# Performance work log

Measured on AMD Instinct MI355X. Metric: run time of the kernel, lower is better.

Reference implementation:

```python
import jax, jax.numpy as jnp
import numpy as np

NUM_HEADS = 8

def _proj(x, w, b):
    # 1x1x1 Conv3d == pointwise linear over channel dim
    return jnp.einsum('bcxyz,oc->boxyz', x, w) + b[None, :, None, None, None]


def setup_inputs() -> dict:
    key = jax.random.key(0)
    ks = jax.random.split(key, 9)
    B, C, X, Y, Z = 2, 256, 48, 48, 48
    s = 0.05
    return {
        'x':  jax.random.normal(ks[0], (B, C, X, Y, Z), dtype=jnp.float32),
        'wq': jax.random.normal(ks[1], (C, C), dtype=jnp.float32) * s,
        'bq': jax.random.normal(ks[2], (C,), dtype=jnp.float32) * s,
        'wk': jax.random.normal(ks[3], (C, C), dtype=jnp.float32) * s,
        'bk': jax.random.normal(ks[4], (C,), dtype=jnp.float32) * s,
        'wv': jax.random.normal(ks[5], (C, C), dtype=jnp.float32) * s,
        'bv': jax.random.normal(ks[6], (C,), dtype=jnp.float32) * s,
        'wo': jax.random.normal(ks[7], (C, C), dtype=jnp.float32) * s,
        'bo': jax.random.normal(ks[8], (C,), dtype=jnp.float32) * s,
    }


def reference(x, wq, bq, wk, bk, wv, bv, wo, bo):
    B, C, X, Y, Z = x.shape
    H = NUM_HEADS
    P = C // H  # per-head channels
    q = _proj(x, wq, bq).reshape(B, H, P, X, Y, Z)
    k = _proj(x, wk, bk).reshape(B, H, P, X, Y, Z)
    v = _proj(x, wv, bv).reshape(B, H, P, X, Y, Z)
    # torch einsum 'bnxyzc,bmxyzc->bnmxy' contracts z and per-head channel c
    scores = jnp.einsum('bncxyz,bmcxyz->bnmxy', q, k) / jnp.sqrt(jnp.float32(P))
    # torch F.softmax(dim=-1) on [b,n,m,x,y] -> softmax over y axis (faithful)
    attn = jax.nn.softmax(scores, axis=-1)
    # torch 'bnmxy,bmxyzc->bnxyzc', then permute/reshape back to [B,C,X,Y,Z]
    out = jnp.einsum('bnmxy,bmcxyz->bncxyz', attn, v).reshape(B, C, X, Y, Z)
    return _proj(out, wo, bo)
```

## Files before the change

kernel.cpp:

```cpp
#include <hip/hip_runtime.h>
#include <hip/hip_bf16.h>
#include <stdint.h>


#define S_TOT 110592
#define NBX   2304

typedef unsigned short u16;
typedef __attribute__((ext_vector_type(8))) short bf16x8;
typedef __attribute__((ext_vector_type(4))) float f32x4;

__device__ __forceinline__ u16 f2b(float f){
  union { float f; uint32_t u; } v; v.f = f;
  uint32_t u = v.u;
  return (u16)((u + 0x7fffu + ((u >> 16) & 1u)) >> 16);
}
__device__ __forceinline__ float b2f(u16 h){
  union { float f; uint32_t u; } v; v.u = ((uint32_t)h) << 16; return v.f;
}
__device__ __forceinline__ f32x4 mfma16(bf16x8 a, bf16x8 b, f32x4 c){
  return __builtin_amdgcn_mfma_f32_16x16x32_bf16(a, b, c, 0, 0, 0);
}

__global__ __launch_bounds__(256) void k_prep(
    const float* __restrict__ wq, const float* __restrict__ wk,
    const float* __restrict__ wv, const float* __restrict__ wo,
    u16* __restrict__ img)
{
  int idx = blockIdx.x * 256 + threadIdx.x;
  if (idx < 131072){
    int ck = idx >> 14, rem = idx & 16383;
    int r = rem >> 5, i = rem & 31;
    int c = ck * 32 + i;
    float v = (r < 256) ? wq[r * 256 + c] : wk[(r - 256) * 256 + c];
    img[idx] = f2b(v);
  } else if (idx < 196608){
    int l = idx - 131072;
    int ck = l >> 13, rem = l & 8191;
    int r = rem >> 5, i = rem & 31;
    img[idx] = f2b(wv[r * 256 + ck * 32 + i]);
  } else if (idx < 262144){
    int l = idx - 196608;
    int ck = l >> 13, rem = l & 8191;
    int r = rem >> 5, i = rem & 31;
    img[idx] = f2b(wo[r * 256 + ck * 32 + i]);
  }
}

#define K1F_LDS 151552
__global__ __launch_bounds__(1024, 4) void k_qkv(
    const float* __restrict__ x, const u16* __restrict__ wimg,
    const u16* __restrict__ wvimg,
    const float* __restrict__ bq, const float* __restrict__ bk,
    const float* __restrict__ bv,
    float* __restrict__ scores, u16* __restrict__ vws)
{
  extern __shared__ char lds[];
  u16* xT  = (u16*)lds;
  u16* qkz = (u16*)(lds + 49152);
  float* ps = (float*)(lds + 147456);

  const int tid  = threadIdx.x;
  const int wave = tid >> 6, lane = tid & 63;
  const int l15 = lane & 15, l4 = lane >> 4;
  const int bx = blockIdx.x, b = blockIdx.y;
  const int s0 = bx * 96;
  const float* xb = x + (size_t)b * 256 * S_TOT;

  #pragma unroll
  for (int it = 0; it < 3; it++){
    int e = it * 1024 + tid;
    int z = e % 96, c16 = e / 96;
    const float* px = xb + (size_t)(c16 * 8) * S_TOT + s0 + z;
    union { uint4 q; u16 h[8]; } u;
    #pragma unroll
    for (int i = 0; i < 8; i++) u.h[i] = f2b(px[(size_t)i * S_TOT]);
    *(uint4*)((char*)xT + z * 512 + ((c16 ^ (z & 7)) << 4)) = u.q;
  }
  __syncthreads();

  const int proj = wave >> 3;
  const int rb = (wave & 7) * 32;
  const float* bias = proj ? bk : bq;

  f32x4 acc[2][6];
  #pragma unroll
  for (int fr = 0; fr < 2; fr++){
    f32x4 iv;
    #pragma unroll
    for (int j = 0; j < 4; j++) iv[j] = bias[rb + fr * 16 + l4 * 4 + j];
    #pragma unroll
    for (int fc = 0; fc < 6; fc++) acc[fr][fc] = iv;
  }
  #pragma unroll
  for (int ck = 0; ck < 8; ck++){
    bf16x8 af[2], bfr[6];
    #pragma unroll
    for (int fr = 0; fr < 2; fr++){
      int row = wave * 32 + fr * 16 + l15;
      af[fr] = *(const bf16x8*)(wimg + ck * 16384 + row * 32 + l4 * 8);
    }
    #pragma unroll
    for (int fc = 0; fc < 6; fc++){
      int z = fc * 16 + l15;
      bfr[fc] = *(const bf16x8*)((char*)xT + z * 512 + (((ck * 4 + l4) ^ (l15 & 7)) << 4));
    }
    #pragma unroll
    for (int fr = 0; fr < 2; fr++)
      #pragma unroll
      for (int fc = 0; fc < 6; fc++)
        acc[fr][fc] = mfma16(af[fr], bfr[fc], acc[fr][fc]);
  }

  #pragma unroll
  for (int fr = 0; fr < 2; fr++){
    int och = proj * 256 + rb + fr * 16 + l4 * 4;
    #pragma unroll
    for (int fc = 0; fc < 6; fc++){
      int z = fc * 16 + l15;
      ushort4 u;
      u.x = f2b(acc[fr][fc][0]); u.y = f2b(acc[fr][fc][1]);
      u.z = f2b(acc[fr][fc][2]); u.w = f2b(acc[fr][fc][3]);
      *(ushort4*)((char*)qkz + z * 1024 + ((((och >> 3) ^ z) & 63) << 4)
                  + (och & 7) * 2) = u;
    }
  }
  __syncthreads();

  {
    const int ca = l15 * 32 + l4 * 8;
    const int cb = 256 + (l15 & 7) * 32 + l4 * 8;
    const int zb = (wave >> 3) * 48 + (wave & 7) * 6;
    f32x4 sc = {0.f, 0.f, 0.f, 0.f};
    #pragma unroll
    for (int zi = 0; zi < 6; zi++){
      int zl = zb + zi;
      bf16x8 aq  = *(const bf16x8*)((char*)qkz + zl * 1024 + ((((ca >> 3) ^ zl) & 63) << 4));
      bf16x8 bk8 = *(const bf16x8*)((char*)qkz + zl * 1024 + ((((cb >> 3) ^ zl) & 63) << 4));
      sc = mfma16(aq, bk8, sc);
    }
    if (l4 < 2 && l15 < 8){
      #pragma unroll
      for (int j = 0; j < 4; j++)
        ps[wave * 64 + (l4 * 4 + j) * 8 + l15] = sc[j];
    }
  }
  __syncthreads();

  if (tid < 128){
    int h = tid >> 6, idx = tid & 63;
    float s = 0.f;
    #pragma unroll
    for (int w = 0; w < 8; w++) s += ps[(h * 8 + w) * 64 + idx];
    scores[(size_t)(b * 64 + idx) * NBX + bx * 2 + h] = s * 0.17677669529663687f;
  }

  f32x4 vac[6];
  {
    f32x4 iv;
    #pragma unroll
    for (int j = 0; j < 4; j++) iv[j] = bv[wave * 16 + l4 * 4 + j];
    #pragma unroll
    for (int fc = 0; fc < 6; fc++) vac[fc] = iv;
  }
  #pragma unroll
  for (int ck = 0; ck < 8; ck++){
    bf16x8 af, bfr[6];
    af = *(const bf16x8*)(wvimg + ck * 8192 + (wave * 16 + l15) * 32 + l4 * 8);
    #pragma unroll
    for (int fc = 0; fc < 6; fc++){
      int z = fc * 16 + l15;
      bfr[fc] = *(const bf16x8*)((char*)xT + z * 512 + (((ck * 4 + l4) ^ (l15 & 7)) << 4));
    }
    #pragma unroll
    for (int fc = 0; fc < 6; fc++)
      vac[fc] = mfma16(af, bfr[fc], vac[fc]);
  }

  {
    u16* vt = vws + (size_t)(b * 1152 + bx) * 24576;
    int ch0 = wave * 16 + l4 * 4;
    #pragma unroll
    for (int fc = 0; fc < 6; fc++){
      int z = fc * 16 + l15;
      ushort4 u;
      u.x = f2b(vac[fc][0]); u.y = f2b(vac[fc][1]);
      u.z = f2b(vac[fc][2]); u.w = f2b(vac[fc][3]);
      *(ushort4*)((char*)vt + z * 512 + ((((ch0 >> 3) ^ (z & 7)) & 31) << 4)
                  + (ch0 & 7) * 2) = u;
    }
  }
}

#define K1_LDS 57344
__global__ __launch_bounds__(1024, 4) void k_qk_scores(
    const float* __restrict__ x, const u16* __restrict__ wimg,
    const float* __restrict__ bq, const float* __restrict__ bk,
    float* __restrict__ scores)
{
  extern __shared__ char lds[];
  u16* xT  = (u16*)lds;
  u16* qkz = (u16*)lds;
  float* ps0 = (float*)(lds + 49152);
  float* ps1 = (float*)(lds + 53248);

  const int tid  = threadIdx.x;
  const int wave = tid >> 6, lane = tid & 63;
  const int l15 = lane & 15, l4 = lane >> 4;
  const int bx = blockIdx.x, b = blockIdx.y;
  const int s0 = bx * 96;
  const float* xb = x + (size_t)b * 256 * S_TOT;

  #pragma unroll
  for (int it = 0; it < 3; it++){
    int e = it * 1024 + tid;
    int z = e % 96, c16 = e / 96;
    const float* px = xb + (size_t)(c16 * 8) * S_TOT + s0 + z;
    union { uint4 q; u16 h[8]; } u;
    #pragma unroll
    for (int i = 0; i < 8; i++) u.h[i] = f2b(px[(size_t)i * S_TOT]);
    *(uint4*)((char*)xT + z * 512 + ((c16 ^ (z & 7)) << 4)) = u.q;
  }
  __syncthreads();

  const int proj = wave >> 3;
  const int rb = (wave & 7) * 32;
  const float* bias = proj ? bk : bq;

  f32x4 acc[2][6];
  #pragma unroll
  for (int fr = 0; fr < 2; fr++){
    f32x4 iv;
    #pragma unroll
    for (int j = 0; j < 4; j++) iv[j] = bias[rb + fr * 16 + l4 * 4 + j];
    #pragma unroll
    for (int fc = 0; fc < 6; fc++) acc[fr][fc] = iv;
  }
  #pragma unroll
  for (int ck = 0; ck < 8; ck++){
    bf16x8 af[2], bfr[6];
    #pragma unroll
    for (int fr = 0; fr < 2; fr++){
      int row = wave * 32 + fr * 16 + l15;
      af[fr] = *(const bf16x8*)(wimg + ck * 16384 + row * 32 + l4 * 8);
    }
    #pragma unroll
    for (int fc = 0; fc < 6; fc++){
      int z = fc * 16 + l15;
      bfr[fc] = *(const bf16x8*)((char*)xT + z * 512 + (((ck * 4 + l4) ^ (l15 & 7)) << 4));
    }
    #pragma unroll
    for (int fr = 0; fr < 2; fr++)
      #pragma unroll
      for (int fc = 0; fc < 6; fc++)
        acc[fr][fc] = mfma16(af[fr], bfr[fc], acc[fr][fc]);
  }
  __syncthreads();

  const int och = proj * 256 + rb + l4 * 4;
  const int ca = l15 * 32 + l4 * 8;
  const int cb = 256 + (l15 & 7) * 32 + l4 * 8;

  #pragma unroll
  for (int fr = 0; fr < 2; fr++){
    int oc = och + fr * 16;
    #pragma unroll
    for (int fc = 0; fc < 3; fc++){
      int zl = fc * 16 + l15;
      ushort4 u;
      u.x = f2b(acc[fr][fc][0]); u.y = f2b(acc[fr][fc][1]);
      u.z = f2b(acc[fr][fc][2]); u.w = f2b(acc[fr][fc][3]);
      *(ushort4*)((char*)qkz + zl * 1024 + ((((oc >> 3) ^ zl) & 63) << 4)
                  + (oc & 7) * 2) = u;
    }
  }
  __syncthreads();
  {
    f32x4 sc = {0.f, 0.f, 0.f, 0.f};
    #pragma unroll
    for (int zi = 0; zi < 3; zi++){
      int zl = wave * 3 + zi;
      bf16x8 aq  = *(const bf16x8*)((char*)qkz + zl * 1024 + ((((ca >> 3) ^ zl) & 63) << 4));
      bf16x8 bk8 = *(const bf16x8*)((char*)qkz + zl * 1024 + ((((cb >> 3) ^ zl) & 63) << 4));
      sc = mfma16(aq, bk8, sc);
    }
    if (l4 < 2 && l15 < 8){
      #pragma unroll
      for (int j = 0; j < 4; j++)
        ps0[wave * 64 + (l4 * 4 + j) * 8 + l15] = sc[j];
    }
  }
  __syncthreads();
  if (tid < 64){
    float s = 0.f;
    #pragma unroll
    for (int w = 0; w < 16; w++) s += ps0[w * 64 + tid];
    scores[(size_t)(b * 64 + tid) * NBX + bx * 2] = s * 0.17677669529663687f;
  }
  #pragma unroll
  for (int fr = 0; fr < 2; fr++){
    int oc = och + fr * 16;
    #pragma unroll
    for (int fc = 3; fc < 6; fc++){
      int zl = (fc - 3) * 16 + l15;
      ushort4 u;
      u.x = f2b(acc[fr][fc][0]); u.y = f2b(acc[fr][fc][1]);
      u.z = f2b(acc[fr][fc][2]); u.w = f2b(acc[fr][fc][3]);
      *(ushort4*)((char*)qkz + zl * 1024 + ((((oc >> 3) ^ zl) & 63) << 4)
                  + (oc & 7) * 2) = u;
    }
  }
  __syncthreads();
  {
    f32x4 sc = {0.f, 0.f, 0.f, 0.f};
    #pragma unroll
    for (int zi = 0; zi < 3; zi++){
      int zl = wave * 3 + zi;
      bf16x8 aq  = *(const bf16x8*)((char*)qkz + zl * 1024 + ((((ca >> 3) ^ zl) & 63) << 4));
      bf16x8 bk8 = *(const bf16x8*)((char*)qkz + zl * 1024 + ((((cb >> 3) ^ zl) & 63) << 4));
      sc = mfma16(aq, bk8, sc);
    }
    if (l4 < 2 && l15 < 8){
      #pragma unroll
      for (int j = 0; j < 4; j++)
        ps1[wave * 64 + (l4 * 4 + j) * 8 + l15] = sc[j];
    }
  }
  __syncthreads();
  if (tid < 64){
    float s = 0.f;
    #pragma unroll
    for (int w = 0; w < 16; w++) s += ps1[w * 64 + tid];
    scores[(size_t)(b * 64 + tid) * NBX + bx * 2 + 1] = s * 0.17677669529663687f;
  }
}

__global__ __launch_bounds__(256) void k_softmax(
    const float* __restrict__ scores, float* __restrict__ attn)
{
  int row  = blockIdx.x * 4 + (threadIdx.x >> 6);
  int lane = threadIdx.x & 63;
  const float* src = scores + (size_t)row * 48;
  float v = (lane < 48) ? src[lane] : -1e30f;
  float m = v;
  #pragma unroll
  for (int off = 32; off; off >>= 1) m = fmaxf(m, __shfl_xor(m, off));
  float e = (lane < 48) ? __expf(v - m) : 0.f;
  float s = e;
  #pragma unroll
  for (int off = 32; off; off >>= 1) s += __shfl_xor(s, off);
  if (lane < 48) attn[(size_t)row * 48 + lane] = e / s;
}

#define K3_LDS 49664
__global__ __launch_bounds__(512, 4) void k_out_v(
    const u16* __restrict__ vws, const u16* __restrict__ woimg,
    const float* __restrict__ bo, const float* __restrict__ attn,
    float* __restrict__ out)
{
  extern __shared__ char lds[];
  u16* vl = (u16*)lds;
  u16* oT = (u16*)lds;
  float* atl = (float*)(lds + 49152);

  const int tid  = threadIdx.x;
  const int wave = tid >> 6, lane = tid & 63;
  const int l15 = lane & 15, l4 = lane >> 4;
  const int bx = blockIdx.x, b = blockIdx.y;
  const int s0 = bx * 96;

  if (tid < 128)
    atl[tid] = attn[(size_t)(b * 64 + (tid & 63)) * NBX + bx * 2 + (tid >> 6)];

  {
    const uint4* vt = (const uint4*)(vws + (size_t)(b * 1152 + bx) * 24576);
    #pragma unroll
    for (int it = 0; it < 6; it++)
      ((uint4*)vl)[it * 512 + tid] = vt[it * 512 + tid];
  }
  __syncthreads();

  #pragma unroll
  for (int it = 0; it < 6; it++){
    int e = it * 512 + tid;
    int c16 = e & 31, z = e >> 5;
    int r = c16 & 3, hn = c16 >> 2;
    const float* at = atl + ((z >= 48) ? 64 : 0);
    float a[8] = {0,0,0,0,0,0,0,0};
    #pragma unroll
    for (int m = 0; m < 8; m++){
      union { uint4 q; u16 h[8]; } v8;
      v8.q = *(const uint4*)((char*)vl + z * 512 + (((m * 4 + r) ^ (z & 7)) << 4));
      float am = at[hn * 8 + m];
      #pragma unroll
      for (int i = 0; i < 8; i++) a[i] = fmaf(am, b2f(v8.h[i]), a[i]);
    }
    union { uint4 q; u16 h[8]; } pk;
    #pragma unroll
    for (int i = 0; i < 8; i++) pk.h[i] = f2b(a[i]);
    __syncthreads();
    *(uint4*)((char*)oT + z * 512 + ((c16 ^ (z & 7)) << 4)) = pk.q;
  }
  __syncthreads();

  f32x4 oac[2][6];
  #pragma unroll
  for (int fr = 0; fr < 2; fr++){
    f32x4 iv;
    #pragma unroll
    for (int j = 0; j < 4; j++) iv[j] = bo[wave * 32 + fr * 16 + l4 * 4 + j];
    #pragma unroll
    for (int fc = 0; fc < 6; fc++) oac[fr][fc] = iv;
  }
  #pragma unroll
  for (int ck = 0; ck < 8; ck++){
    bf16x8 af[2], bfr[6];
    #pragma unroll
    for (int fr = 0; fr < 2; fr++){
      int row = wave * 32 + fr * 16 + l15;
      af[fr] = *(const bf16x8*)(woimg + ck * 8192 + row * 32 + l4 * 8);
    }
    #pragma unroll
    for (int fc = 0; fc < 6; fc++){
      int z = fc * 16 + l15;
      bfr[fc] = *(const bf16x8*)((char*)oT + z * 512 + (((ck * 4 + l4) ^ (l15 & 7)) << 4));
    }
    #pragma unroll
    for (int fr = 0; fr < 2; fr++)
      #pragma unroll
      for (int fc = 0; fc < 6; fc++)
        oac[fr][fc] = mfma16(af[fr], bfr[fc], oac[fr][fc]);
  }

  #pragma unroll
  for (int fr = 0; fr < 2; fr++)
    #pragma unroll
    for (int fc = 0; fc < 6; fc++)
      #pragma unroll
      for (int j = 0; j < 4; j++){
        int o = wave * 32 + fr * 16 + l4 * 4 + j;
        int z = fc * 16 + l15;
        __builtin_nontemporal_store(oac[fr][fc][j],
            &out[(size_t)(b * 256 + o) * S_TOT + s0 + z]);
      }
}

__global__ __launch_bounds__(512, 4) void k_out(
    const float* __restrict__ x, const u16* __restrict__ wvimg,
    const u16* __restrict__ woimg, const float* __restrict__ bv,
    const float* __restrict__ bo, const float* __restrict__ attn,
    float* __restrict__ out)
{
  extern __shared__ char lds[];
  u16* xT = (u16*)lds;
  u16* vl = (u16*)lds;
  u16* oT = (u16*)lds;
  float* atl = (float*)(lds + 49152);

  const int tid  = threadIdx.x;
  const int wave = tid >> 6, lane = tid & 63;
  const int l15 = lane & 15, l4 = lane >> 4;
  const int bx = blockIdx.x, b = blockIdx.y;
  const int s0 = bx * 96;
  const float* xb = x + (size_t)b * 256 * S_TOT;

  if (tid < 128)
    atl[tid] = attn[(size_t)(b * 64 + (tid & 63)) * NBX + bx * 2 + (tid >> 6)];

  #pragma unroll
  for (int it = 0; it < 6; it++){
    int e = it * 512 + tid;
    int z = e % 96, c16 = e / 96;
    const float* px = xb + (size_t)(c16 * 8) * S_TOT + s0 + z;
    union { uint4 q; u16 h[8]; } u;
    #pragma unroll
    for (int i = 0; i < 8; i++) u.h[i] = f2b(px[(size_t)i * S_TOT]);
    *(uint4*)((char*)xT + z * 512 + ((c16 ^ (z & 7)) << 4)) = u.q;
  }
  __syncthreads();

  f32x4 vac[2][6];
  #pragma unroll
  for (int fr = 0; fr < 2; fr++){
    f32x4 iv;
    #pragma unroll
    for (int j = 0; j < 4; j++) iv[j] = bv[wave * 32 + fr * 16 + l4 * 4 + j];
    #pragma unroll
    for (int fc = 0; fc < 6; fc++) vac[fr][fc] = iv;
  }
  #pragma unroll
  for (int ck = 0; ck < 8; ck++){
    bf16x8 af[2], bfr[6];
    #pragma unroll
    for (int fr = 0; fr < 2; fr++){
      int row = wave * 32 + fr * 16 + l15;
      af[fr] = *(const bf16x8*)(wvimg + ck * 8192 + row * 32 + l4 * 8);
    }
    #pragma unroll
    for (int fc = 0; fc < 6; fc++){
      int z = fc * 16 + l15;
      bfr[fc] = *(const bf16x8*)((char*)xT + z * 512 + (((ck * 4 + l4) ^ (l15 & 7)) << 4));
    }
    #pragma unroll
    for (int fr = 0; fr < 2; fr++)
      #pragma unroll
      for (int fc = 0; fc < 6; fc++)
        vac[fr][fc] = mfma16(af[fr], bfr[fc], vac[fr][fc]);
  }
  __syncthreads();

  #pragma unroll
  for (int fr = 0; fr < 2; fr++){
    int o0 = wave * 32 + fr * 16 + l4 * 4;
    #pragma unroll
    for (int fc = 0; fc < 6; fc++){
      int z = fc * 16 + l15;
      ushort4 u;
      u.x = f2b(vac[fr][fc][0]); u.y = f2b(vac[fr][fc][1]);
      u.z = f2b(vac[fr][fc][2]); u.w = f2b(vac[fr][fc][3]);
      *(ushort4*)((char*)vl + z * 512 + (((o0 >> 3) ^ (z & 7)) << 4) + (o0 & 7) * 2) = u;
    }
  }
  __syncthreads();

  #pragma unroll
  for (int it = 0; it < 6; it++){
    int e = it * 512 + tid;
    int c16 = e & 31, z = e >> 5;
    int r = c16 & 3, hn = c16 >> 2;
    const float* at = atl + ((z >= 48) ? 64 : 0);
    float a[8] = {0,0,0,0,0,0,0,0};
    #pragma unroll
    for (int m = 0; m < 8; m++){
      union { uint4 q; u16 h[8]; } v8;
      v8.q = *(const uint4*)((char*)vl + z * 512 + (((m * 4 + r) ^ (z & 7)) << 4));
      float am = at[hn * 8 + m];
      #pragma unroll
      for (int i = 0; i < 8; i++) a[i] = fmaf(am, b2f(v8.h[i]), a[i]);
    }
    union { uint4 q; u16 h[8]; } pk;
    #pragma unroll
    for (int i = 0; i < 8; i++) pk.h[i] = f2b(a[i]);
    __syncthreads();
    *(uint4*)((char*)oT + z * 512 + ((c16 ^ (z & 7)) << 4)) = pk.q;
  }
  __syncthreads();

  f32x4 oac[2][6];
  #pragma unroll
  for (int fr = 0; fr < 2; fr++){
    f32x4 iv;
    #pragma unroll
    for (int j = 0; j < 4; j++) iv[j] = bo[wave * 32 + fr * 16 + l4 * 4 + j];
    #pragma unroll
    for (int fc = 0; fc < 6; fc++) oac[fr][fc] = iv;
  }
  #pragma unroll
  for (int ck = 0; ck < 8; ck++){
    bf16x8 af[2], bfr[6];
    #pragma unroll
    for (int fr = 0; fr < 2; fr++){
      int row = wave * 32 + fr * 16 + l15;
      af[fr] = *(const bf16x8*)(woimg + ck * 8192 + row * 32 + l4 * 8);
    }
    #pragma unroll
    for (int fc = 0; fc < 6; fc++){
      int z = fc * 16 + l15;
      bfr[fc] = *(const bf16x8*)((char*)oT + z * 512 + (((ck * 4 + l4) ^ (l15 & 7)) << 4));
    }
    #pragma unroll
    for (int fr = 0; fr < 2; fr++)
      #pragma unroll
      for (int fc = 0; fc < 6; fc++)
        oac[fr][fc] = mfma16(af[fr], bfr[fc], oac[fr][fc]);
  }

  #pragma unroll
  for (int fr = 0; fr < 2; fr++)
    #pragma unroll
    for (int fc = 0; fc < 6; fc++)
      #pragma unroll
      for (int j = 0; j < 4; j++){
        int o = wave * 32 + fr * 16 + l4 * 4 + j;
        int z = fc * 16 + l15;
        __builtin_nontemporal_store(oac[fr][fc][j],
            &out[(size_t)(b * 256 + o) * S_TOT + s0 + z]);
      }
}

extern "C" void kernel_launch(void* const* d_in, const int* in_sizes, int n_in,
                              void* d_out, int out_size, void* d_ws, size_t ws_size,
                              hipStream_t stream) {
  (void)in_sizes; (void)n_in; (void)out_size;
  const float* x  = (const float*)d_in[0];
  const float* wq = (const float*)d_in[1];
  const float* bq = (const float*)d_in[2];
  const float* wk = (const float*)d_in[3];
  const float* bk = (const float*)d_in[4];
  const float* wv = (const float*)d_in[5];
  const float* bv = (const float*)d_in[6];
  const float* wo = (const float*)d_in[7];
  const float* bo = (const float*)d_in[8];
  float* out = (float*)d_out;

  char* ws = (char*)d_ws;
  u16*  wimg   = (u16*)ws;
  u16*  wvimg  = wimg + 131072;
  u16*  woimg  = wimg + 196608;
  float* scores = (float*)(ws + 524288);
  float* attn   = (float*)(ws + 1703936);
  u16*  vws     = (u16*)(ws + 2883584);

  const size_t need = 2883584 + 113246208;
  const bool fused = (ws_size >= need);

  k_prep<<<1024, 256, 0, stream>>>(wq, wk, wv, wo, wimg);
  if (fused){
    hipFuncSetAttribute((const void*)k_qkv,
                        hipFuncAttributeMaxDynamicSharedMemorySize, K1F_LDS);
    k_qkv<<<dim3(1152, 2), 1024, K1F_LDS, stream>>>(
        x, wimg, wvimg, bq, bk, bv, scores, vws);
  } else {
    k_qk_scores<<<dim3(1152, 2), 1024, K1_LDS, stream>>>(x, wimg, bq, bk, scores);
  }
  k_softmax<<<1536, 256, 0, stream>>>(scores, attn);
  if (fused){
    k_out_v<<<dim3(1152, 2), 512, K3_LDS, stream>>>(vws, woimg, bo, attn, out);
  } else {
    k_out<<<dim3(1152, 2), 512, K3_LDS, stream>>>(
        x, wvimg, woimg, bv, bo, attn, out);
  }
}
```

Measured before the change: 231.2 us.

## Move V projection to output kernel and cache bf16 x tile in workspace

The fused QKV kernel, which needed a large LDS footprint, is removed. The smaller QK-scores kernel now writes its transposed bf16 x tile to the workspace with nontemporal stores. The output kernel reads that tile back and computes the V projection itself before applying attention and the output projection. The goal is to cut LDS use and raise occupancy in the first kernel while keeping the fp32 x reread out of the last kernel. The cost is moving V-projection MFMA work into the output kernel, with the same workspace traffic as before.

```diff
diff --git a/kernel.cpp b/kernel.cpp
--- a/kernel.cpp
+++ b/kernel.cpp
@@ -9,6 +9,7 @@
 typedef unsigned short u16;
 typedef __attribute__((ext_vector_type(8))) short bf16x8;
 typedef __attribute__((ext_vector_type(4))) float f32x4;
+typedef __attribute__((ext_vector_type(4))) uint32_t u32x4;
 
 __device__ __forceinline__ u16 f2b(float f){
   union { float f; uint32_t u; } v; v.f = f;
@@ -47,18 +48,17 @@
   }
 }
 
-#define K1F_LDS 151552
-__global__ __launch_bounds__(1024, 4) void k_qkv(
+#define K1_LDS 57344
+__global__ __launch_bounds__(1024, 4) void k_qk_scores(
     const float* __restrict__ x, const u16* __restrict__ wimg,
-    const u16* __restrict__ wvimg,
     const float* __restrict__ bq, const float* __restrict__ bk,
-    const float* __restrict__ bv,
-    float* __restrict__ scores, u16* __restrict__ vws)
+    float* __restrict__ scores, u16* __restrict__ xws)
 {
   extern __shared__ char lds[];
   u16* xT  = (u16*)lds;
-  u16* qkz = (u16*)(lds + 49152);
-  float* ps = (float*)(lds + 147456);
+  u16* qkz = (u16*)lds;
+  float* ps0 = (float*)(lds + 49152);
+  float* ps1 = (float*)(lds + 53248);
 
   const int tid  = threadIdx.x;
   const int wave = tid >> 6, lane = tid & 63;
@@ -66,160 +66,19 @@
   const int bx = blockIdx.x, b = blockIdx.y;
   const int s0 = bx * 96;
   const float* xb = x + (size_t)b * 256 * S_TOT;
+  u16* vt = xws ? (xws + (size_t)(b * 1152 + bx) * 24576) : (u16*)0;
 
   #pragma unroll
   for (int it = 0; it < 3; it++){
     int e = it * 1024 + tid;
     int z = e % 96, c16 = e / 96;
     const float* px = xb + (size_t)(c16 * 8) * S_TOT + s0 + z;
-    union { uint4 q; u16 h[8]; } u;
+    union { u32x4 q; u16 h[8]; } u;
     #pragma unroll
     for (int i = 0; i < 8; i++) u.h[i] = f2b(px[(size_t)i * S_TOT]);
-    *(uint4*)((char*)xT + z * 512 + ((c16 ^ (z & 7)) << 4)) = u.q;
-  }
-  __syncthreads();
-
-  const int proj = wave >> 3;
-  const int rb = (wave & 7) * 32;
-  const float* bias = proj ? bk : bq;
-
-  f32x4 acc[2][6];
-  #pragma unroll
-  for (int fr = 0; fr < 2; fr++){
-    f32x4 iv;
-    #pragma unroll
-    for (int j = 0; j < 4; j++) iv[j] = bias[rb + fr * 16 + l4 * 4 + j];
-    #pragma unroll
-    for (int fc = 0; fc < 6; fc++) acc[fr][fc] = iv;
-  }
-  #pragma unroll
-  for (int ck = 0; ck < 8; ck++){
-    bf16x8 af[2], bfr[6];
-    #pragma unroll
-    for (int fr = 0; fr < 2; fr++){
-      int row = wave * 32 + fr * 16 + l15;
-      af[fr] = *(const bf16x8*)(wimg + ck * 16384 + row * 32 + l4 * 8);
-    }
-    #pragma unroll
-    for (int fc = 0; fc < 6; fc++){
-      int z = fc * 16 + l15;
-      bfr[fc] = *(const bf16x8*)((char*)xT + z * 512 + (((ck * 4 + l4) ^ (l15 & 7)) << 4));
-    }
-    #pragma unroll
-    for (int fr = 0; fr < 2; fr++)
-      #pragma unroll
-      for (int fc = 0; fc < 6; fc++)
-        acc[fr][fc] = mfma16(af[fr], bfr[fc], acc[fr][fc]);
-  }
-
-  #pragma unroll
-  for (int fr = 0; fr < 2; fr++){
-    int och = proj * 256 + rb + fr * 16 + l4 * 4;
-    #pragma unroll
-    for (int fc = 0; fc < 6; fc++){
-      int z = fc * 16 + l15;
-      ushort4 u;
-      u.x = f2b(acc[fr][fc][0]); u.y = f2b(acc[fr][fc][1]);
-      u.z = f2b(acc[fr][fc][2]); u.w = f2b(acc[fr][fc][3]);
-      *(ushort4*)((char*)qkz + z * 1024 + ((((och >> 3) ^ z) & 63) << 4)
-                  + (och & 7) * 2) = u;
-    }
-  }
-  __syncthreads();
-
-  {
-    const int ca = l15 * 32 + l4 * 8;
-    const int cb = 256 + (l15 & 7) * 32 + l4 * 8;
-    const int zb = (wave >> 3) * 48 + (wave & 7) * 6;
-    f32x4 sc = {0.f, 0.f, 0.f, 0.f};
-    #pragma unroll
-    for (int zi = 0; zi < 6; zi++){
-      int zl = zb + zi;
-      bf16x8 aq  = *(const bf16x8*)((char*)qkz + zl * 1024 + ((((ca >> 3) ^ zl) & 63) << 4));
-      bf16x8 bk8 = *(const bf16x8*)((char*)qkz + zl * 1024 + ((((cb >> 3) ^ zl) & 63) << 4));
-      sc = mfma16(aq, bk8, sc);
-    }
-    if (l4 < 2 && l15 < 8){
-      #pragma unroll
-      for (int j = 0; j < 4; j++)
-        ps[wave * 64 + (l4 * 4 + j) * 8 + l15] = sc[j];
-    }
-  }
-  __syncthreads();
-
-  if (tid < 128){
-    int h = tid >> 6, idx = tid & 63;
-    float s = 0.f;
-    #pragma unroll
-    for (int w = 0; w < 8; w++) s += ps[(h * 8 + w) * 64 + idx];
-    scores[(size_t)(b * 64 + idx) * NBX + bx * 2 + h] = s * 0.17677669529663687f;
-  }
-
-  f32x4 vac[6];
-  {
-    f32x4 iv;
-    #pragma unroll
-    for (int j = 0; j < 4; j++) iv[j] = bv[wave * 16 + l4 * 4 + j];
-    #pragma unroll
-    for (int fc = 0; fc < 6; fc++) vac[fc] = iv;
-  }
-  #pragma unroll
-  for (int ck = 0; ck < 8; ck++){
-    bf16x8 af, bfr[6];
-    af = *(const bf16x8*)(wvimg + ck * 8192 + (wave * 16 + l15) * 32 + l4 * 8);
-    #pragma unroll
-    for (int fc = 0; fc < 6; fc++){
-      int z = fc * 16 + l15;
-      bfr[fc] = *(const bf16x8*)((char*)xT + z * 512 + (((ck * 4 + l4) ^ (l15 & 7)) << 4));
-    }
-    #pragma unroll
-    for (int fc = 0; fc < 6; fc++)
-      vac[fc] = mfma16(af, bfr[fc], vac[fc]);
-  }
-
-  {
-    u16* vt = vws + (size_t)(b * 1152 + bx) * 24576;
-    int ch0 = wave * 16 + l4 * 4;
-    #pragma unroll
-    for (int fc = 0; fc < 6; fc++){
-      int z = fc * 16 + l15;
-      ushort4 u;
-      u.x = f2b(vac[fc][0]); u.y = f2b(vac[fc][1]);
-      u.z = f2b(vac[fc][2]); u.w = f2b(vac[fc][3]);
-      *(ushort4*)((char*)vt + z * 512 + ((((ch0 >> 3) ^ (z & 7)) & 31) << 4)
-                  + (ch0 & 7) * 2) = u;
-    }
-  }
-}
-
-#define K1_LDS 57344
-__global__ __launch_bounds__(1024, 4) void k_qk_scores(
-    const float* __restrict__ x, const u16* __restrict__ wimg,
-    const float* __restrict__ bq, const float* __restrict__ bk,
-    float* __restrict__ scores)
-{
-  extern __shared__ char lds[];
-  u16* xT  = (u16*)lds;
-  u16* qkz = (u16*)lds;
-  float* ps0 = (float*)(lds + 49152);
-  float* ps1 = (float*)(lds + 53248);
-
-  const int tid  = threadIdx.x;
-  const int wave = tid >> 6, lane = tid & 63;
-  const int l15 = lane & 15, l4 = lane >> 4;
-  const int bx = blockIdx.x, b = blockIdx.y;
-  const int s0 = bx * 96;
-  const float* xb = x + (size_t)b * 256 * S_TOT;
-
-  #pragma unroll
-  for (int it = 0; it < 3; it++){
-    int e = it * 1024 + tid;
-    int z = e % 96, c16 = e / 96;
-    const float* px = xb + (size_t)(c16 * 8) * S_TOT + s0 + z;
-    union { uint4 q; u16 h[8]; } u;
-    #pragma unroll
-    for (int i = 0; i < 8; i++) u.h[i] = f2b(px[(size_t)i * S_TOT]);
-    *(uint4*)((char*)xT + z * 512 + ((c16 ^ (z & 7)) << 4)) = u.q;
+    int off = z * 512 + ((c16 ^ (z & 7)) << 4);
+    *(u32x4*)((char*)xT + off) = u.q;
+    if (vt) __builtin_nontemporal_store(u.q, (u32x4*)((char*)vt + off));
   }
   __syncthreads();
 
@@ -291,6 +150,7 @@
     }
   }
   __syncthreads();
+
   if (tid < 64){
     float s = 0.f;
     #pragma unroll
@@ -353,12 +213,14 @@
 }
 
 #define K3_LDS 49664
-__global__ __launch_bounds__(512, 4) void k_out_v(
-    const u16* __restrict__ vws, const u16* __restrict__ woimg,
+__global__ __launch_bounds__(512, 4) void k_out_x(
+    const u16* __restrict__ xws, const u16* __restrict__ wvimg,
+    const u16* __restrict__ woimg, const float* __restrict__ bv,
     const float* __restrict__ bo, const float* __restrict__ attn,
     float* __restrict__ out)
 {
   extern __shared__ char lds[];
+  u16* xT = (u16*)lds;
   u16* vl = (u16*)lds;
   u16* oT = (u16*)lds;
   float* atl = (float*)(lds + 49152);
@@ -373,10 +235,54 @@
     atl[tid] = attn[(size_t)(b * 64 + (tid & 63)) * NBX + bx * 2 + (tid >> 6)];
 
   {
-    const uint4* vt = (const uint4*)(vws + (size_t)(b * 1152 + bx) * 24576);
+    const u32x4* vt = (const u32x4*)(xws + (size_t)(b * 1152 + bx) * 24576);
     #pragma unroll
     for (int it = 0; it < 6; it++)
-      ((uint4*)vl)[it * 512 + tid] = vt[it * 512 + tid];
+      ((u32x4*)xT)[it * 512 + tid] = __builtin_nontemporal_load(&vt[it * 512 + tid]);
+  }
+  __syncthreads();
+
+  f32x4 vac[2][6];
+  #pragma unroll
+  for (int fr = 0; fr < 2; fr++){
+    f32x4 iv;
+    #pragma unroll
+    for (int j = 0; j < 4; j++) iv[j] = bv[wave * 32 + fr * 16 + l4 * 4 + j];
+    #pragma unroll
+    for (int fc = 0; fc < 6; fc++) vac[fr][fc] = iv;
+  }
+  #pragma unroll
+  for (int ck = 0; ck < 8; ck++){
+    bf16x8 af[2], bfr[6];
+    #pragma unroll
+    for (int fr = 0; fr < 2; fr++){
+      int row = wave * 32 + fr * 16 + l15;
+      af[fr] = *(const bf16x8*)(wvimg + ck * 8192 + row * 32 + l4 * 8);
+    }
+    #pragma unroll
+    for (int fc = 0; fc < 6; fc++){
+      int z = fc * 16 + l15;
+      bfr[fc] = *(const bf16x8*)((char*)xT + z * 512 + (((ck * 4 + l4) ^ (l15 & 7)) << 4));
+    }
+    #pragma unroll
+    for (int fr = 0; fr < 2; fr++)
+      #pragma unroll
+      for (int fc = 0; fc < 6; fc++)
+        vac[fr][fc] = mfma16(af[fr], bfr[fc], vac[fr][fc]);
+  }
+  __syncthreads();
+
+  #pragma unroll
+  for (int fr = 0; fr < 2; fr++){
+    int o0 = wave * 32 + fr * 16 + l4 * 4;
+    #pragma unroll
+    for (int fc = 0; fc < 6; fc++){
+      int z = fc * 16 + l15;
+      ushort4 u;
+      u.x = f2b(vac[fr][fc][0]); u.y = f2b(vac[fr][fc][1]);
+      u.z = f2b(vac[fr][fc][2]); u.w = f2b(vac[fr][fc][3]);
+      *(ushort4*)((char*)vl + z * 512 + (((o0 >> 3) ^ (z & 7)) << 4) + (o0 & 7) * 2) = u;
+    }
   }
   __syncthreads();
 
@@ -609,23 +515,18 @@
   u16*  woimg  = wimg + 196608;
   float* scores = (float*)(ws + 524288);
   float* attn   = (float*)(ws + 1703936);
-  u16*  vws     = (u16*)(ws + 2883584);
+  u16*  xws     = (u16*)(ws + 2883584);
 
   const size_t need = 2883584 + 113246208;
   const bool fused = (ws_size >= need);
 
   k_prep<<<1024, 256, 0, stream>>>(wq, wk, wv, wo, wimg);
-  if (fused){
-    hipFuncSetAttribute((const void*)k_qkv,
-                        hipFuncAttributeMaxDynamicSharedMemorySize, K1F_LDS);
-    k_qkv<<<dim3(1152, 2), 1024, K1F_LDS, stream>>>(
-        x, wimg, wvimg, bq, bk, bv, scores, vws);
-  } else {
-    k_qk_scores<<<dim3(1152, 2), 1024, K1_LDS, stream>>>(x, wimg, bq, bk, scores);
-  }
+  k_qk_scores<<<dim3(1152, 2), 1024, K1_LDS, stream>>>(
+      x, wimg, bq, bk, scores, fused ? xws : (u16*)nullptr);
   k_softmax<<<1536, 256, 0, stream>>>(scores, attn);
   if (fused){
-    k_out_v<<<dim3(1152, 2), 512, K3_LDS, stream>>>(vws, woimg, bo, attn, out);
+    k_out_x<<<dim3(1152, 2), 512, K3_LDS, stream>>>(
+        xws, wvimg, woimg, bv, bo, attn, out);
   } else {
     k_out<<<dim3(1152, 2), 512, K3_LDS, stream>>>(
         x, wvimg, woimg, bv, bo, attn, out);
```

Measured after the change: 370.3 us. +60.2%, slower.
